# Kernel tuning notes

Measured on AMD Instinct MI355X. Metric: run time of the kernel, lower is better.

Reference implementation:

```python
import jax, jax.numpy as jnp
import numpy as np

WARMUP = 5

def _smooth_l1(x):
    a = jnp.abs(x)
    return jnp.where(a < 1.0, 0.5 * a * a, a - 0.5)


def setup_inputs() -> dict:
    key = jax.random.key(0)
    ks = jax.random.split(key, 6)
    B, S, N, M, C = 8, 4, 8192, 50, 10
    return dict(
        pred_boxes=jax.random.normal(ks[0], (B, S, N, 7), jnp.float32),
        pred_classes=jax.random.normal(ks[1], (B, S, N, C), jnp.float32),
        pred_scores=jax.random.normal(ks[2], (B, S, N), jnp.float32),
        gt_boxes=jax.random.normal(ks[3], (B, M, 7), jnp.float32) * 3.0,
        gt_classes=jax.random.randint(ks[4], (B, M), 0, C),
        n_gt=jax.random.randint(ks[5], (B,), 1, M + 1),
        w_center=jnp.float32(2.0),   # loss_weights['center']
        w_obj=jnp.float32(0.5),      # loss_weights['obj']
        w_unmatched=jnp.float32(5.0),# loss_weights['unmatched']
        epoch=0,
    )


def _forward(pred_boxes, pred_classes, pred_scores, gt_boxes, gt_classes, n_gt, w_center, w_obj, w_unmatched, epoch):
    # epoch < WARMUP path: k_factor=10, use_objectness=False, distance_threshold=5.0, cls_weight=0
    K_FACTOR = 10
    COST_THRESH = 5.0 * 10.0  # distance_threshold * 10
    B, S, N, _ = pred_boxes.shape
    M = gt_boxes.shape[1]
    gt_mask = jnp.arange(M)[None, :] < n_gt[:, None]            # [B,M] valid (non-padded) GTs

    pc = pred_boxes[..., :3]                                    # [B,S,N,3]
    gc = gt_boxes[..., :3]                                      # [B,M,3]
    diff = pc[:, :, :, None, :] - gc[:, None, None, :, :]       # [B,S,N,M,3]
    dist = jnp.sqrt(jnp.sum(diff * diff, axis=-1))              # [B,S,N,M] center L2 cost

    # ---- progressive matching (vectorized over B,S,GT) ----
    cost = jnp.where(gt_mask[:, None, None, :], dist, jnp.inf)
    masked = jnp.where(cost < COST_THRESH, cost, jnp.inf)
    neg = -jnp.swapaxes(masked, -1, -2)                         # [B,S,M,N]
    vals, idx = jax.lax.top_k(neg, K_FACTOR)                    # k smallest costs per gt
    pick_ok = vals > -jnp.inf                                   # [B,S,M,k] valid picks
    gt_ids = jnp.broadcast_to(jnp.arange(M, dtype=jnp.int32)[None, None, :, None], idx.shape)
    bidx = jnp.broadcast_to(jnp.arange(B)[:, None, None, None], idx.shape)
    sidx = jnp.broadcast_to(jnp.arange(S)[None, :, None, None], idx.shape)
    assign = jnp.full((B, S, N), -1, dtype=jnp.int32)
    assign = assign.at[bidx, sidx, idx].max(jnp.where(pick_ok, gt_ids, -1))
    matched_gt = pick_ok.any(-1)                                # [B,S,M]
    unmatched = gt_mask[:, None, :] & ~matched_gt               # [B,S,M]

    # ---- center loss (smooth-L1 over matched query/GT center pairs) ----
    pos = assign >= 0                                           # [B,S,N]
    a = jnp.maximum(assign, 0)
    gtc = gc[jnp.arange(B)[:, None, None], a]                   # [B,S,N,3]
    n_pos = pos.sum().astype(jnp.float32)
    loss_center = jnp.sum(_smooth_l1(pc - gtc) * pos[..., None]) / jnp.maximum(n_pos * 3.0, 1.0)

    # ---- progressive objectness loss (BCE-with-logits + dynamic pos_weight) ----
    t = pos.astype(pred_scores.dtype)
    n_neg = jnp.float32(t.size) - n_pos
    pw = jnp.minimum(10.0, n_neg / jnp.maximum(n_pos, 1.0))     # epoch < warmup branch
    x = pred_scores
    loss_obj = jnp.mean(pw * t * jax.nn.softplus(-x) + (1.0 - t) * jax.nn.softplus(x))

    # ---- unmatched-GT loss: pull 5 nearest predictions toward each unmatched GT ----
    dist_t = jnp.swapaxes(dist, -1, -2)                         # [B,S,M,N]
    nd, ni = jax.lax.top_k(-dist_t, 5)
    nd = -nd                                                    # 5 smallest distances [B,S,M,5]
    b5 = jnp.broadcast_to(jnp.arange(B)[:, None, None, None], ni.shape)
    s5 = jnp.broadcast_to(jnp.arange(S)[None, :, None, None], ni.shape)
    obj5 = pred_scores[b5, s5, ni]                              # [B,S,M,5]
    per_gt = jnp.mean(jnp.exp(-nd / 2.0) * (1.0 - obj5), axis=-1)
    per_gt = jnp.where(unmatched, per_gt, 0.0)
    n_entries = jnp.sum(unmatched.any(-1)).astype(jnp.float32)  # number of (b,s) pairs with unmatched gts
    loss_unm = per_gt.sum() / jnp.maximum(n_entries, 1.0)

    return loss_center * w_center + loss_obj * w_obj + loss_unm * w_unmatched


def reference(pred_boxes, pred_classes, pred_scores, gt_boxes, gt_classes, n_gt, w_center, w_obj, w_unmatched, epoch):
    return _forward(pred_boxes, pred_classes, pred_scores, gt_boxes, gt_classes, n_gt, w_center, w_obj, w_unmatched, epoch)
```

## Files before the change

kernel.cpp:

```cpp
#include <hip/hip_runtime.h>

#define NB 8
#define NS 4
#define NN 8192
#define NM 50
#define K10 10
#define COST_THRESH 50.0f
#define LOSS_BLOCKS 256
#define NBUCK 1024
#define NSUB 4
#define CAP 256
#define TOTAL (NB * NS * NN)
#define TT 512
#define ELEMS (NN / TT)

__device__ __forceinline__ bool lexless(float d1, int i1, float d2, int i2) {
  return (d1 < d2) || (d1 == d2 && i1 < i2);
}

__global__ void __launch_bounds__(256) prep_kernel(
    const float* __restrict__ pred_boxes, float* __restrict__ packed,
    int* __restrict__ assign, float* __restrict__ acc,
    int* __restrict__ bs_unm, int* __restrict__ done) {
  int i = blockIdx.x * blockDim.x + threadIdx.x;
  for (int j = i; j < TOTAL; j += gridDim.x * blockDim.x) {
    assign[j] = -1;
    packed[j] = pred_boxes[j * 7 + 0];
    packed[TOTAL + j] = pred_boxes[j * 7 + 1];
    packed[2 * TOTAL + j] = pred_boxes[j * 7 + 2];
  }
  if (i == 0) { acc[0] = 0.0f; *done = 0; }
  if (i >= 64 && i < 64 + NB * NS) bs_unm[i - 64] = 0;
}

__global__ void __launch_bounds__(TT) topk_kernel(
    const float* __restrict__ packed, const float* __restrict__ pred_scores,
    const float* __restrict__ gt_boxes, const int* __restrict__ n_gt,
    int* __restrict__ assign, float* __restrict__ per_gt_sum,
    int* __restrict__ bs_unm) {
  const int blk = blockIdx.x;
  const int m = blk % NM;
  const int bs = blk / NM;
  const int b = bs / NS;
  const int t = threadIdx.x;

  __shared__ int shist[NSUB][NBUCK];
  __shared__ float scd[CAP];
  __shared__ int sci[CAP];
  __shared__ float sred[16];
  __shared__ float sbb[2];
  __shared__ int scnt;
  __shared__ int sbucket;
  __shared__ float soutd[K10];
  __shared__ int souti[K10];

  for (int i = t; i < NSUB * NBUCK; i += TT) ((int*)shist)[i] = 0;
  if (t == 0) { scnt = 0; sbucket = NBUCK - 2; }

  const float gx = gt_boxes[(b * NM + m) * 7 + 0];
  const float gy = gt_boxes[(b * NM + m) * 7 + 1];
  const float gz = gt_boxes[(b * NM + m) * 7 + 2];
  const bool valid = (m < n_gt[b]);

  const float4* px4 = (const float4*)(packed + (size_t)bs * NN);
  const float4* py4 = (const float4*)(packed + TOTAL + (size_t)bs * NN);
  const float4* pz4 = (const float4*)(packed + 2 * TOTAL + (size_t)bs * NN);

  float d2r[ELEMS];
  float lmin = INFINITY, lmax = 0.0f;
#pragma unroll
  for (int c = 0; c < ELEMS / 4; c++) {
    float4 vx = px4[c * TT + t];
    float4 vy = py4[c * TT + t];
    float4 vz = pz4[c * TT + t];
    float dx, dy, dz;
    dx = vx.x - gx; dy = vy.x - gy; dz = vz.x - gz; d2r[c * 4 + 0] = dx * dx + dy * dy + dz * dz;
    dx = vx.y - gx; dy = vy.y - gy; dz = vz.y - gz; d2r[c * 4 + 1] = dx * dx + dy * dy + dz * dz;
    dx = vx.z - gx; dy = vy.z - gy; dz = vz.z - gz; d2r[c * 4 + 2] = dx * dx + dy * dy + dz * dz;
    dx = vx.w - gx; dy = vy.w - gy; dz = vz.w - gz; d2r[c * 4 + 3] = dx * dx + dy * dy + dz * dz;
#pragma unroll
    for (int j = 0; j < 4; j++) {
      lmin = fminf(lmin, d2r[c * 4 + j]);
      lmax = fmaxf(lmax, d2r[c * 4 + j]);
    }
  }
#pragma unroll
  for (int off = 32; off >= 1; off >>= 1) {
    lmin = fminf(lmin, __shfl_down(lmin, off));
    lmax = fmaxf(lmax, __shfl_down(lmax, off));
  }
  const int wave = t >> 6;
  if ((t & 63) == 0) { sred[wave] = lmin; sred[8 + wave] = lmax; }
  __syncthreads();
  if (t == 0) {
    float bmin = INFINITY, bmax = 0.0f;
#pragma unroll
    for (int w = 0; w < TT / 64; w++) {
      bmin = fminf(bmin, sred[w]);
      bmax = fmaxf(bmax, sred[8 + w]);
    }
    sbb[0] = bmin;
    sbb[1] = (float)NBUCK / fmaxf(bmax - bmin, 1e-30f);
  }
  __syncthreads();
  const float bmin = sbb[0], scale = sbb[1];

  int* hist = shist[wave & (NSUB - 1)];
#pragma unroll
  for (int e = 0; e < ELEMS; e++) {
    int bidx = (int)((d2r[e] - bmin) * scale);
    bidx = min(NBUCK - 1, max(0, bidx));
    atomicAdd(&hist[bidx], 1);
  }
  __syncthreads();
  for (int i = t; i < NBUCK; i += TT)
    shist[0][i] += shist[1][i] + shist[2][i] + shist[3][i];
  __syncthreads();

  if (t < 64) {
    int lsum = 0;
    for (int i = 0; i < NBUCK / 64; i++) lsum += shist[0][t * (NBUCK / 64) + i];
    int incl = lsum;
#pragma unroll
    for (int off = 1; off < 64; off <<= 1) {
      int v = __shfl_up(incl, off);
      if (t >= off) incl += v;
    }
    int excl = incl - lsum;
    if (excl < K10 && incl >= K10) {
      int c = excl;
      for (int i = 0; i < NBUCK / 64; i++) {
        c += shist[0][t * (NBUCK / 64) + i];
        if (c >= K10) { sbucket = t * (NBUCK / 64) + i; break; }
      }
    }
  }
  __syncthreads();
  const float bound = bmin + ((float)(sbucket + 2) + 0.5f) / scale;

#pragma unroll
  for (int c = 0; c < ELEMS / 4; c++) {
#pragma unroll
    for (int j = 0; j < 4; j++) {
      float d2 = d2r[c * 4 + j];
      if (d2 < bound) {
        int p = atomicAdd(&scnt, 1);
        if (p < CAP) { scd[p] = d2; sci[p] = (c * TT + t) * 4 + j; }
      }
    }
  }
  __syncthreads();
  const int K = min(scnt, CAP);

  for (int c = t; c < K; c += TT) scd[c] = sqrtf(scd[c]);
  __syncthreads();
  for (int c = t; c < K; c += TT) {
    float dc = scd[c];
    int ic = sci[c];
    int rank = 0;
    for (int o = 0; o < K; o++) rank += lexless(scd[o], sci[o], dc, ic) ? 1 : 0;
    if (rank < K10) { soutd[rank] = dc; souti[rank] = ic; }
  }
  __syncthreads();

  if (t < 64) {
    bool pick = (t < K10) && valid && (soutd[t] < COST_THRESH);
    if (pick) atomicMax(&assign[(size_t)bs * NN + souti[t]], m);
    bool matched = __any(pick);
    if (valid && !matched) {
      float a = 0.0f;
      if (t < 5) a = expf(-0.5f * soutd[t]) * (1.0f - pred_scores[(size_t)bs * NN + souti[t]]);
#pragma unroll
      for (int off = 8; off >= 1; off >>= 1) a += __shfl_down(a, off);
      if (t == 0) {
        atomicAdd(per_gt_sum, a * 0.2f);
        atomicOr(&bs_unm[bs], 1);
      }
    }
  }
}

__global__ void __launch_bounds__(256) loss_final_kernel(
    const float* __restrict__ packed, const float* __restrict__ pred_scores,
    const float* __restrict__ gt_boxes, const int* __restrict__ assign,
    float* __restrict__ partials, int* __restrict__ done,
    const float* __restrict__ acc, const int* __restrict__ bs_unm,
    const float* __restrict__ wc, const float* __restrict__ wo,
    const float* __restrict__ wu, float* __restrict__ out) {
  int tid = blockIdx.x * blockDim.x + threadIdx.x;
  float lc = 0.0f, spp = 0.0f, spn = 0.0f, np = 0.0f;
  for (int i = tid; i < TOTAL; i += gridDim.x * blockDim.x) {
    int a = assign[i];
    float x = pred_scores[i];
    if (a >= 0) {
      np += 1.0f;
      int b = i / (NS * NN);
      const float* gbp = &gt_boxes[(b * NM + a) * 7];
#pragma unroll
      for (int c = 0; c < 3; c++) {
        float diff = packed[c * TOTAL + i] - gbp[c];
        float ad = fabsf(diff);
        lc += (ad < 1.0f) ? 0.5f * ad * ad : (ad - 0.5f);
      }
      spp += log1pf(expf(-fabsf(x))) + fmaxf(-x, 0.0f);
    } else {
      spn += log1pf(expf(-fabsf(x))) + fmaxf(x, 0.0f);
    }
  }
#pragma unroll
  for (int off = 32; off >= 1; off >>= 1) {
    lc += __shfl_down(lc, off);
    spp += __shfl_down(spp, off);
    spn += __shfl_down(spn, off);
    np += __shfl_down(np, off);
  }
  __shared__ float red[4][4];
  __shared__ int s_last;
  int wave = threadIdx.x >> 6;
  if ((threadIdx.x & 63) == 0) {
    red[wave][0] = lc; red[wave][1] = spp; red[wave][2] = spn; red[wave][3] = np;
  }
  __syncthreads();
  if (threadIdx.x == 0) {
    float o0 = 0, o1 = 0, o2 = 0, o3 = 0;
#pragma unroll
    for (int w = 0; w < 4; w++) { o0 += red[w][0]; o1 += red[w][1]; o2 += red[w][2]; o3 += red[w][3]; }
    float* p = &partials[(size_t)blockIdx.x * 8];
    __hip_atomic_store(&p[0], o0, __ATOMIC_RELAXED, __HIP_MEMORY_SCOPE_AGENT);
    __hip_atomic_store(&p[1], o1, __ATOMIC_RELAXED, __HIP_MEMORY_SCOPE_AGENT);
    __hip_atomic_store(&p[2], o2, __ATOMIC_RELAXED, __HIP_MEMORY_SCOPE_AGENT);
    __hip_atomic_store(&p[3], o3, __ATOMIC_RELAXED, __HIP_MEMORY_SCOPE_AGENT);
    __threadfence();
    int ticket = __hip_atomic_fetch_add(done, 1, __ATOMIC_ACQ_REL, __HIP_MEMORY_SCOPE_AGENT);
    s_last = (ticket == gridDim.x - 1) ? 1 : 0;
  }
  __syncthreads();
  if (s_last) {
    __threadfence();
    const int t = threadIdx.x;
    float l0 = __hip_atomic_load(&partials[t * 8 + 0], __ATOMIC_RELAXED, __HIP_MEMORY_SCOPE_AGENT);
    float l1 = __hip_atomic_load(&partials[t * 8 + 1], __ATOMIC_RELAXED, __HIP_MEMORY_SCOPE_AGENT);
    float l2 = __hip_atomic_load(&partials[t * 8 + 2], __ATOMIC_RELAXED, __HIP_MEMORY_SCOPE_AGENT);
    float l3 = __hip_atomic_load(&partials[t * 8 + 3], __ATOMIC_RELAXED, __HIP_MEMORY_SCOPE_AGENT);
#pragma unroll
    for (int off = 32; off >= 1; off >>= 1) {
      l0 += __shfl_down(l0, off);
      l1 += __shfl_down(l1, off);
      l2 += __shfl_down(l2, off);
      l3 += __shfl_down(l3, off);
    }
    __shared__ float red2[4][4];
    if ((t & 63) == 0) {
      red2[t >> 6][0] = l0; red2[t >> 6][1] = l1; red2[t >> 6][2] = l2; red2[t >> 6][3] = l3;
    }
    __syncthreads();
    if (t == 0) {
      float o0 = 0, o1 = 0, o2 = 0, o3 = 0;
#pragma unroll
      for (int w = 0; w < 4; w++) { o0 += red2[w][0]; o1 += red2[w][1]; o2 += red2[w][2]; o3 += red2[w][3]; }
      int ne = 0;
      for (int i = 0; i < NB * NS; i++) ne += bs_unm[i];
      float n_pos = o3;
      float loss_center = o0 / fmaxf(n_pos * 3.0f, 1.0f);
      float n_neg = (float)TOTAL - n_pos;
      float pw = fminf(10.0f, n_neg / fmaxf(n_pos, 1.0f));
      float loss_obj = (pw * o1 + o2) / (float)TOTAL;
      float loss_unm = acc[0] / fmaxf((float)ne, 1.0f);
      out[0] = loss_center * wc[0] + loss_obj * wo[0] + loss_unm * wu[0];
    }
  }
}

extern "C" void kernel_launch(void* const* d_in, const int* in_sizes, int n_in,
                              void* d_out, int out_size, void* d_ws, size_t ws_size,
                              hipStream_t stream) {
  const float* pred_boxes = (const float*)d_in[0];
  const float* pred_scores = (const float*)d_in[2];
  const float* gt_boxes = (const float*)d_in[3];
  const int* n_gt = (const int*)d_in[5];
  const float* wc = (const float*)d_in[6];
  const float* wo = (const float*)d_in[7];
  const float* wu = (const float*)d_in[8];
  float* out = (float*)d_out;

  char* ws = (char*)d_ws;
  int* assign = (int*)ws;
  float* packed = (float*)(ws + (size_t)TOTAL * 4);
  float* acc = (float*)(ws + (size_t)TOTAL * 16);
  int* done = (int*)((char*)acc + 64);
  int* bs_unm = (int*)((char*)acc + 128);
  float* partials = (float*)((char*)acc + 512);

  prep_kernel<<<512, 256, 0, stream>>>(pred_boxes, packed, assign, acc, bs_unm, done);
  topk_kernel<<<NB * NS * NM, TT, 0, stream>>>(packed, pred_scores, gt_boxes,
                                               n_gt, assign, &acc[0], bs_unm);
  loss_final_kernel<<<LOSS_BLOCKS, 256, 0, stream>>>(packed, pred_scores, gt_boxes, assign,
                                                     partials, done, acc, bs_unm, wc, wo, wu, out);
}
```

Baseline: 46.49 us.

## Replace histogram threshold search with count-based bisection and ballot compaction

```diff
diff --git a/kernel.cpp b/kernel.cpp
--- a/kernel.cpp
+++ b/kernel.cpp
@@ -7,9 +7,8 @@
 #define K10 10
 #define COST_THRESH 50.0f
 #define LOSS_BLOCKS 256
-#define NBUCK 1024
-#define NSUB 4
-#define CAP 256
+#define CAP 1024
+#define CAP_HI 128
 #define TOTAL (NB * NS * NN)
 #define TT 512
 #define ELEMS (NN / TT)
@@ -33,7 +32,7 @@
   if (i >= 64 && i < 64 + NB * NS) bs_unm[i - 64] = 0;
 }
 
-__global__ void __launch_bounds__(TT) topk_kernel(
+__global__ void __launch_bounds__(TT, 4) topk_kernel(
     const float* __restrict__ packed, const float* __restrict__ pred_scores,
     const float* __restrict__ gt_boxes, const int* __restrict__ n_gt,
     int* __restrict__ assign, float* __restrict__ per_gt_sum,
@@ -43,19 +42,19 @@
   const int bs = blk / NM;
   const int b = bs / NS;
   const int t = threadIdx.x;
-
-  __shared__ int shist[NSUB][NBUCK];
+  const int wave = t >> 6;
+  const int lane = t & 63;
+
   __shared__ float scd[CAP];
   __shared__ int sci[CAP];
-  __shared__ float sred[16];
+  __shared__ float sred[2][8];
   __shared__ float sbb[2];
+  __shared__ int scount[2][8];
   __shared__ int scnt;
-  __shared__ int sbucket;
   __shared__ float soutd[K10];
   __shared__ int souti[K10];
 
-  for (int i = t; i < NSUB * NBUCK; i += TT) ((int*)shist)[i] = 0;
-  if (t == 0) { scnt = 0; sbucket = NBUCK - 2; }
+  if (t == 0) scnt = 0;
 
   const float gx = gt_boxes[(b * NM + m) * 7 + 0];
   const float gy = gt_boxes[(b * NM + m) * 7 + 1];
@@ -89,64 +88,56 @@
     lmin = fminf(lmin, __shfl_down(lmin, off));
     lmax = fmaxf(lmax, __shfl_down(lmax, off));
   }
-  const int wave = t >> 6;
-  if ((t & 63) == 0) { sred[wave] = lmin; sred[8 + wave] = lmax; }
+  if (lane == 0) { sred[0][wave] = lmin; sred[1][wave] = lmax; }
   __syncthreads();
   if (t == 0) {
     float bmin = INFINITY, bmax = 0.0f;
 #pragma unroll
     for (int w = 0; w < TT / 64; w++) {
-      bmin = fminf(bmin, sred[w]);
-      bmax = fmaxf(bmax, sred[8 + w]);
+      bmin = fminf(bmin, sred[0][w]);
+      bmax = fmaxf(bmax, sred[1][w]);
     }
     sbb[0] = bmin;
-    sbb[1] = (float)NBUCK / fmaxf(bmax - bmin, 1e-30f);
-  }
-  __syncthreads();
-  const float bmin = sbb[0], scale = sbb[1];
-
-  int* hist = shist[wave & (NSUB - 1)];
+    sbb[1] = bmax;
+  }
+  __syncthreads();
+
+  float lo = sbb[0];
+  float hi = sbb[1] * 1.000001f + 1e-30f;
+  float bound = hi;
+  int buf = 0;
+  for (int iter = 0; iter < 32; iter++) {
+    float mid = 0.5f * (lo + hi);
+    int c = 0;
+#pragma unroll
+    for (int e = 0; e < ELEMS; e++) c += (d2r[e] < mid) ? 1 : 0;
+#pragma unroll
+    for (int off = 32; off >= 1; off >>= 1) c += __shfl_down(c, off);
+    if (lane == 0) scount[buf][wave] = c;
+    __syncthreads();
+    int C = 0;
+#pragma unroll
+    for (int w = 0; w < TT / 64; w++) C += scount[buf][w];
+    buf ^= 1;
+    bool collapsed = (mid <= lo) || (mid >= hi);
+    if (C >= K10 && (C <= CAP_HI || collapsed)) { bound = mid; break; }
+    if (collapsed) { bound = hi; break; }
+    if (C < K10) lo = mid; else hi = mid;
+  }
+
 #pragma unroll
   for (int e = 0; e < ELEMS; e++) {
-    int bidx = (int)((d2r[e] - bmin) * scale);
-    bidx = min(NBUCK - 1, max(0, bidx));
-    atomicAdd(&hist[bidx], 1);
-  }
-  __syncthreads();
-  for (int i = t; i < NBUCK; i += TT)
-    shist[0][i] += shist[1][i] + shist[2][i] + shist[3][i];
-  __syncthreads();
-
-  if (t < 64) {
-    int lsum = 0;
-    for (int i = 0; i < NBUCK / 64; i++) lsum += shist[0][t * (NBUCK / 64) + i];
-    int incl = lsum;
-#pragma unroll
-    for (int off = 1; off < 64; off <<= 1) {
-      int v = __shfl_up(incl, off);
-      if (t >= off) incl += v;
-    }
-    int excl = incl - lsum;
-    if (excl < K10 && incl >= K10) {
-      int c = excl;
-      for (int i = 0; i < NBUCK / 64; i++) {
-        c += shist[0][t * (NBUCK / 64) + i];
-        if (c >= K10) { sbucket = t * (NBUCK / 64) + i; break; }
-      }
-    }
-  }
-  __syncthreads();
-  const float bound = bmin + ((float)(sbucket + 2) + 0.5f) / scale;
-
-#pragma unroll
-  for (int c = 0; c < ELEMS / 4; c++) {
-#pragma unroll
-    for (int j = 0; j < 4; j++) {
-      float d2 = d2r[c * 4 + j];
-      if (d2 < bound) {
-        int p = atomicAdd(&scnt, 1);
-        if (p < CAP) { scd[p] = d2; sci[p] = (c * TT + t) * 4 + j; }
-      }
+    int n = (e < ELEMS ? ((e >> 2) * TT + t) * 4 + (e & 3) : 0);
+    bool p = d2r[e] < bound;
+    unsigned long long mask = __ballot(p);
+    if (mask) {
+      int leader = __ffsll((long long)mask) - 1;
+      int cnt = __popcll(mask);
+      int base = 0;
+      if (lane == leader) base = atomicAdd(&scnt, cnt);
+      base = __shfl(base, leader);
+      int pos = base + __popcll(mask & ((1ull << lane) - 1ull));
+      if (p && pos < CAP) { scd[pos] = d2r[e]; sci[pos] = n; }
     }
   }
   __syncthreads();
```

Measured after the change: 53.63 us. 15.3% more time.
